# Performance work log

Hardware: AMD Instinct MI355X
Metric: run time of the kernel (lower is better)

## Reference

```python
import jax, jax.numpy as jnp
import numpy as np

N, E, G = 20000, 320000, 128
L, D, De, Fa, Ff = 3, 64, 32, 92, 128
IN = 2 * D + De  # 160


def setup_inputs() -> dict:
    key = jax.random.key(0)
    ks = jax.random.split(key, 12)
    s = 0.05
    return {
        "atom_features": jax.random.normal(ks[0], (N, Fa), jnp.float32),
        "bondlength": jax.random.uniform(ks[1], (E,), jnp.float32) * 8.0,
        "src": jax.random.randint(ks[2], (E,), 0, N, dtype=jnp.int32),
        "dst": jax.random.randint(ks[3], (E,), 0, N, dtype=jnp.int32),
        "graph_id": jnp.sort(jax.random.randint(ks[4], (N,), 0, G, dtype=jnp.int32)),
        "emb_W": jax.random.normal(ks[5], (Fa, D), jnp.float32) * s,
        "emb_b": jnp.zeros((D,), jnp.float32),
        "Wi": jax.random.normal(ks[6], (L, IN, D), jnp.float32) * s,
        "bi": jnp.zeros((L, D), jnp.float32),
        "gi": jnp.ones((L, D), jnp.float32),
        "bbi": jnp.zeros((L, D), jnp.float32),
        "Wu": jax.random.normal(ks[7], (L, IN, D), jnp.float32) * s,
        "bu": jnp.zeros((L, D), jnp.float32),
        "gu": jnp.ones((L, D), jnp.float32),
        "bbu": jnp.zeros((L, D), jnp.float32),
        "gn": jnp.ones((L, D), jnp.float32),
        "bbn": jnp.zeros((L, D), jnp.float32),
        "fc_W": jax.random.normal(ks[8], (D, Ff), jnp.float32) * s,
        "fc_b": jnp.zeros((Ff,), jnp.float32),
        "out_W": jax.random.normal(ks[9], (Ff, 1), jnp.float32) * s,
        "out_b": jnp.zeros((1,), jnp.float32),
    }


def _bn(x, g, b, eps=1e-5):
    # BatchNorm1d in training mode: biased batch statistics over axis 0
    mu = x.mean(axis=0)
    var = x.var(axis=0)
    return g * (x - mu) * jax.lax.rsqrt(var + eps) + b


def _rbf(d):
    centers = jnp.linspace(0.0, 8.0, De)
    gamma = 1.0 / (8.0 / (De - 1))  # 1 / mean center spacing (alignn default)
    return jnp.exp(-gamma * (d[:, None] - centers) ** 2)  # [E, De]


def reference(atom_features, bondlength, src, dst, graph_id,
              emb_W, emb_b, Wi, bi, gi, bbi, Wu, bu, gu, bbu, gn, bbn,
              fc_W, fc_b, out_W, out_b):
    sp = jax.nn.softplus
    edge_feats = _rbf(bondlength)                       # [E, De]
    h = atom_features @ emb_W + emb_b                   # [N, D]
    for l in range(L):
        z = jnp.concatenate([h[src], h[dst], edge_feats], axis=1)  # [E, 160]
        gate = jax.nn.sigmoid(_bn(z @ Wi[l] + bi[l], gi[l], bbi[l]))
        upd = sp(_bn(z @ Wu[l] + bu[l], gu[l], bbu[l]))
        m = jax.ops.segment_sum(gate * upd, dst, num_segments=N)   # [N, D]
        h = sp(h + _bn(m, gn[l], bbn[l]))
    # AvgPooling over graphs
    sums = jax.ops.segment_sum(h, graph_id, num_segments=G)       # [G, D]
    cnt = jax.ops.segment_sum(jnp.ones((N,), h.dtype), graph_id, num_segments=G)
    feats = sums / jnp.maximum(cnt, 1.0)[:, None]
    feats = sp(feats)
    feats = sp(feats @ fc_W + fc_b)   # Linear + Softplus (self.fc)
    feats = sp(feats)
    out = feats @ out_W + out_b       # [G, 1], identity link
    return jnp.squeeze(out, axis=-1)  # [G]
```

## Files before the change

kernel.cpp:

```cpp
#include <hip/hip_runtime.h>
#include <hip/hip_bf16.h>
#include <math.h>

#define NN 20000
#define NE 320000
#define NG 128
#define DD 64
#define FA 92
#define FF 128
#define NT (NE / 16)
#define NBLK 2500
#define NAB 1250
#define NHB 625
#define GAMMA 3.875f
#define CEN (8.0f / 31.0f)
#define L2E 1.44269504f
#define RBF2 (-GAMMA * L2E)

typedef __attribute__((ext_vector_type(8))) short bf16x8;
typedef __attribute__((ext_vector_type(4))) float f32x4;


__device__ __forceinline__ float sp_(float x) {
    return fmaxf(x, 0.f) + __logf(1.f + __expf(-fabsf(x)));
}
__device__ __forceinline__ unsigned short f2b(float x) {
    __hip_bfloat16 b = __float2bfloat16(x);
    return *reinterpret_cast<unsigned short*>(&b);
}
__device__ __forceinline__ float b2f(unsigned short u) {
    return __uint_as_float((unsigned)u << 16);
}

__device__ __forceinline__ float tree16(float v[16], int r) {
#pragma unroll
    for (int m = 1; m < 16; m <<= 1) {
        bool b = (r & m) != 0;
        int cnt = 8 / m;
#pragma unroll
        for (int i = 0; i < cnt; ++i) {
            float keep = b ? v[2 * i + 1] : v[2 * i];
            float disc = b ? v[2 * i] : v[2 * i + 1];
            float recv = __shfl_xor(disc, m, 64);
            v[i] = keep + recv;
        }
    }
    return v[0];
}

__global__ __launch_bounds__(256) void embed_k(const float* __restrict__ af,
                                               const float* __restrict__ W,
                                               const float* __restrict__ b,
                                               float* __restrict__ h,
                                               unsigned short* __restrict__ hb) {
    __shared__ float Ws[FA * DD];
    __shared__ float afS[32][FA];
    const int n0 = blockIdx.x * 32;
    for (int i = threadIdx.x * 4; i < FA * DD; i += 256 * 4)
        *(float4*)&Ws[i] = *(const float4*)&W[i];
    const float4* af4 = (const float4*)(af + (size_t)n0 * FA);
    for (int i = threadIdx.x; i < 32 * FA / 4; i += 256) {
        float4 v = af4[i];
        int nl = i / (FA / 4), kk = (i % (FA / 4)) * 4;
        *(float4*)&afS[nl][kk] = v;
    }
    __syncthreads();
    int nl = threadIdx.x >> 3, ch = threadIdx.x & 7;
    int n = n0 + nl;
    float acc[8];
#pragma unroll
    for (int q = 0; q < 8; ++q) acc[q] = b[ch * 8 + q];
#pragma unroll 4
    for (int k = 0; k < FA; ++k) {
        float a = afS[nl][k];
        const float* wr = &Ws[k * DD + ch * 8];
        float4 w0 = *(const float4*)wr;
        float4 w1 = *(const float4*)(wr + 4);
        acc[0] += a * w0.x; acc[1] += a * w0.y; acc[2] += a * w0.z; acc[3] += a * w0.w;
        acc[4] += a * w1.x; acc[5] += a * w1.y; acc[6] += a * w1.z; acc[7] += a * w1.w;
    }
    float* o = h + (size_t)n * DD + ch * 8;
    float4 o0, o1;
    o0.x = acc[0]; o0.y = acc[1]; o0.z = acc[2]; o0.w = acc[3];
    o1.x = acc[4]; o1.y = acc[5]; o1.z = acc[6]; o1.w = acc[7];
    *(float4*)o = o0;
    *(float4*)(o + 4) = o1;
    bf16x8 hb8;
#pragma unroll
    for (int q = 0; q < 8; ++q) hb8[q] = (short)f2b(acc[q]);
    *(bf16x8*)(hb + (size_t)n * DD + ch * 8) = hb8;
}

__global__ void prep_wf_k(const float* __restrict__ Wi, const float* __restrict__ Wu,
                          unsigned short* __restrict__ Wf) {
    int b = blockIdx.x;
    int l = b >> 1, g = b & 1;
    const float* W = (g ? Wu : Wi) + (size_t)l * 160 * DD;
    for (int f = threadIdx.x; f < 10240; f += 256) {
        int i = f & 7;
        int lane = (f >> 3) & 63;
        int nf = (f >> 9) & 3;
        int kt = f >> 11;
        int k = kt * 32 + 8 * (lane >> 4) + i;
        int col = nf * 16 + (lane & 15);
        Wf[(size_t)b * 10240 + f] = f2b(W[k * DD + col]);
    }
}

__global__ void cnt_edges_k(const int* __restrict__ src, const int* __restrict__ dst,
                            int* __restrict__ icnt, int* __restrict__ ocnt) {
    int e = blockIdx.x * 256 + threadIdx.x;
    if (e < NE) {
        atomicAdd(&icnt[dst[e]], 1);
        atomicAdd(&ocnt[src[e]], 1);
    }
}

__global__ __launch_bounds__(1024) void csr_scan_k(const int* __restrict__ cnt,
                                                   int* __restrict__ off,
                                                   int* __restrict__ cur) {
    __shared__ int part[1024];
    int t = threadIdx.x;
    int base = t * 20;
    int s = 0;
    for (int i = 0; i < 20; ++i) { int idx = base + i; if (idx < NN) s += cnt[idx]; }
    part[t] = s;
    __syncthreads();
    for (int ofs = 1; ofs < 1024; ofs <<= 1) {
        int v = (t >= ofs) ? part[t - ofs] : 0;
        __syncthreads();
        part[t] += v;
        __syncthreads();
    }
    int run = (t == 0) ? 0 : part[t - 1];
    for (int i = 0; i < 20; ++i) {
        int idx = base + i;
        if (idx < NN) { off[idx] = run; cur[idx] = run; run += cnt[idx]; }
    }
    if (t == 1023) off[NN] = run;
}

__global__ void fill_edges_k(const int* __restrict__ src, const int* __restrict__ dst,
                             const float* __restrict__ bond,
                             int* __restrict__ cur, int* __restrict__ ssrc,
                             int* __restrict__ sdst, float* __restrict__ bond_s) {
    int e = blockIdx.x * 256 + threadIdx.x;
    if (e < NE) {
        int d = dst[e];
        int p = atomicAdd(&cur[d], 1);
        ssrc[p] = src[e];
        sdst[p] = d;
        bond_s[p] = bond[e];
    }
}

__global__ __launch_bounds__(256) void rbfsum_k(const float* __restrict__ bond,
                                                float* __restrict__ zr) {
    __shared__ float part[4][32];
    int lane = threadIdx.x & 63;
    int w = threadIdx.x >> 6;
    int col = lane & 31;
    int half = lane >> 5;
    int slot = (blockIdx.x * 4 + w) * 2 + half;
    int nslots = gridDim.x * 8;
    float cen = (float)col * CEN;
    float a = 0.f;
    for (int e = slot; e < NE; e += nslots) {
        float u = bond[e] - cen;
        a += b2f(f2b(__builtin_amdgcn_exp2f(u * u * RBF2)));
    }
    a += __shfl_xor(a, 32, 64);
    if (half == 0) part[w][col] = a;
    __syncthreads();
    if (threadIdx.x < 32) {
        float s = part[0][threadIdx.x] + part[1][threadIdx.x] +
                  part[2][threadIdx.x] + part[3][threadIdx.x];
        unsafeAtomicAdd(&zr[threadIdx.x], s);
    }
}

__global__ __launch_bounds__(256) void zsum_node_k(const unsigned short* __restrict__ hb,
                                                   const int* __restrict__ ocnt,
                                                   const int* __restrict__ icnt,
                                                   float* __restrict__ zS,
                                                   float* __restrict__ zD) {
    int t = blockIdx.x * 256 + threadIdx.x;
    int col = t & 63;
    int n0 = t >> 6;
    int nstride = (gridDim.x * 256) >> 6;
    float aS = 0.f, aD = 0.f;
    for (int n = n0; n < NN; n += nstride) {
        float v = b2f(hb[(size_t)n * DD + col]);
        aS += (float)ocnt[n] * v;
        aD += (float)icnt[n] * v;
    }
    unsafeAtomicAdd(&zS[col], aS);
    unsafeAtomicAdd(&zD[col], aD);
}

__global__ __launch_bounds__(512, 8) void edge_pre3_k(const unsigned short* __restrict__ hb,
                                                      const float* __restrict__ bond_s,
                                                      const unsigned short* __restrict__ Wf,
                                                      const int* __restrict__ ssrc,
                                                      const int* __restrict__ sdst,
                                                      unsigned short* __restrict__ preIb,
                                                      unsigned short* __restrict__ preUb,
                                                      float* __restrict__ pq) {
    __shared__ bf16x8 WfS[2560];
    float* qred = (float*)WfS;
    const int bidx = blockIdx.x;
    const int lane = threadIdx.x & 63;
    const int w = threadIdx.x >> 6;
    const int r = lane & 15;
    const int c = lane >> 4;
    const int tile = bidx * 8 + w;
    const int e = tile * 16 + r;

    int es = ssrc[e];
    int ed = sdst[e];
    float bd = bond_s[e];
    bf16x8 a0 = *(const bf16x8*)(hb + (size_t)es * DD + c * 8);
    bf16x8 a1 = *(const bf16x8*)(hb + (size_t)es * DD + 32 + c * 8);
    bf16x8 a2 = *(const bf16x8*)(hb + (size_t)ed * DD + c * 8);
    bf16x8 a3 = *(const bf16x8*)(hb + (size_t)ed * DD + 32 + c * 8);
    bf16x8 a4;
#pragma unroll
    for (int i = 0; i < 8; ++i) {
        float u = bd - (float)(8 * c + i) * CEN;
        a4[i] = (short)f2b(__builtin_amdgcn_exp2f(u * u * RBF2));
    }

    {
        const bf16x8* Wf8 = (const bf16x8*)Wf;
        for (int i = threadIdx.x; i < 2560; i += 512) WfS[i] = Wf8[i];
    }
    __syncthreads();

    float qI[16], qU[16];
    {
        f32x4 acc[4];
#pragma unroll
        for (int nf = 0; nf < 4; ++nf) { f32x4 z4 = {0.f, 0.f, 0.f, 0.f}; acc[nf] = z4; }
#pragma unroll
        for (int kt = 0; kt < 5; ++kt) {
            bf16x8 a = (kt == 0) ? a0 : (kt == 1) ? a1 : (kt == 2) ? a2 : (kt == 3) ? a3 : a4;
#pragma unroll
            for (int nf = 0; nf < 4; ++nf)
                acc[nf] = __builtin_amdgcn_mfma_f32_16x16x32_bf16(WfS[(kt * 4 + nf) * 64 + lane], a, acc[nf], 0, 0, 0);
        }
        unsigned short* pre = preIb + (size_t)e * DD + c * 4;
#pragma unroll
        for (int nf = 0; nf < 4; ++nf) {
            ushort4 o;
            o.x = f2b(acc[nf][0]); o.y = f2b(acc[nf][1]);
            o.z = f2b(acc[nf][2]); o.w = f2b(acc[nf][3]);
            *(ushort4*)(pre + nf * 16) = o;
#pragma unroll
            for (int j = 0; j < 4; ++j) qI[nf * 4 + j] = acc[nf][j] * acc[nf][j];
        }
    }
    {
        f32x4 acc[4];
#pragma unroll
        for (int nf = 0; nf < 4; ++nf) { f32x4 z4 = {0.f, 0.f, 0.f, 0.f}; acc[nf] = z4; }
#pragma unroll
        for (int kt = 0; kt < 5; ++kt) {
            bf16x8 a = (kt == 0) ? a0 : (kt == 1) ? a1 : (kt == 2) ? a2 : (kt == 3) ? a3 : a4;
#pragma unroll
            for (int nf = 0; nf < 4; ++nf)
                acc[nf] = __builtin_amdgcn_mfma_f32_16x16x32_bf16(WfS[1280 + (kt * 4 + nf) * 64 + lane], a, acc[nf], 0, 0, 0);
        }
        unsigned short* pre = preUb + (size_t)e * DD + c * 4;
#pragma unroll
        for (int nf = 0; nf < 4; ++nf) {
            ushort4 o;
            o.x = f2b(acc[nf][0]); o.y = f2b(acc[nf][1]);
            o.z = f2b(acc[nf][2]); o.w = f2b(acc[nf][3]);
            *(ushort4*)(pre + nf * 16) = o;
#pragma unroll
            for (int j = 0; j < 4; ++j) qU[nf * 4 + j] = acc[nf][j] * acc[nf][j];
        }
    }

    float vI = tree16(qI, r);
    float vU = tree16(qU, r);
    int col = (r >> 2) * 16 + c * 4 + (r & 3);
    __syncthreads();
    qred[w * 128 + col] = vI;
    qred[w * 128 + 64 + col] = vU;
    __syncthreads();
    if (threadIdx.x < 128) {
        float s8 = 0.f;
#pragma unroll
        for (int ww = 0; ww < 8; ++ww) s8 += qred[ww * 128 + threadIdx.x];
        pq[(size_t)threadIdx.x * NBLK + bidx] = s8;
    }
}

__global__ __launch_bounds__(256) void red2_k(const float* __restrict__ pq,
                                              const float* __restrict__ zpart,
                                              float* __restrict__ stats, int withz) {
    __shared__ float red[256];
    int b = blockIdx.x;
    const float* row;
    float* out;
    int len;
    if (b < 128) { row = pq + (size_t)b * NBLK; out = &stats[b]; len = NBLK; }
    else {
        if (!withz) return;
        row = zpart + (size_t)(b - 128) * NHB; out = &stats[256 + (b - 128)]; len = NHB;
    }
    float s = 0.f;
    for (int i = threadIdx.x; i < len; i += 256) s += row[i];
    red[threadIdx.x] = s;
    __syncthreads();
    for (int ofs = 128; ofs >= 1; ofs >>= 1) {
        if (threadIdx.x < ofs) red[threadIdx.x] += red[threadIdx.x + ofs];
        __syncthreads();
    }
    if (threadIdx.x == 0) *out = red[0];
}

__global__ __launch_bounds__(256) void fin_iu_k(const float* __restrict__ stats,
                                                const unsigned short* __restrict__ Wf,
                                                const float* __restrict__ gi, const float* __restrict__ bbi,
                                                const float* __restrict__ gu, const float* __restrict__ bbu,
                                                float* __restrict__ coeff) {
    __shared__ float redI[256], redU[256];
    int t = threadIdx.x;
    int j = t & 63, part = t >> 6;
    int nf = j >> 4, rr = j & 15;
    float muI = 0.f, muU = 0.f;
    for (int k = part; k < 160; k += 4) {
        float zs = (k < 128) ? stats[256 + k] : stats[384 + k - 128];
        int kt = k >> 5, rem = k & 31, cc = rem >> 3, ii = rem & 7;
        int f = kt * 2048 + nf * 512 + (cc * 16 + rr) * 8 + ii;
        muI += zs * b2f(Wf[f]);
        muU += zs * b2f(Wf[10240 + f]);
    }
    redI[t] = muI;
    redU[t] = muU;
    __syncthreads();
    if (t < 64) {
        muI = redI[t] + redI[64 + t] + redI[128 + t] + redI[192 + t];
        muU = redU[t] + redU[64 + t] + redU[128 + t] + redU[192 + t];
        const float invE = 1.f / (float)NE;
        muI *= invE; muU *= invE;
        float varI = stats[t] * invE - muI * muI;
        float sI = gi[t] * rsqrtf(varI + 1e-5f);
        float tI = bbi[t] - muI * sI;
        float varU = stats[64 + t] * invE - muU * muU;
        float sU = gu[t] * rsqrtf(varU + 1e-5f);
        float tU = bbu[t] - muU * sU;
        coeff[t]       = -L2E * sI;
        coeff[64 + t]  = -L2E * tI;
        coeff[128 + t] =  L2E * sU;
        coeff[192 + t] =  L2E * tU;
    }
}

__global__ __launch_bounds__(256) void apply_node_k(const unsigned short* __restrict__ preIb,
                                                    const unsigned short* __restrict__ preUb,
                                                    const int* __restrict__ eoff,
                                                    const float* __restrict__ coeff,
                                                    float* __restrict__ m,
                                                    float* __restrict__ mpart) {
    __shared__ float ps[128][8];
    __shared__ float pq2[128][8];
    int ch = threadIdx.x & 7;
    int half = (threadIdx.x >> 3) & 1;
    int nl = threadIdx.x >> 4;
    int n = blockIdx.x * 16 + nl;
    float sIv[8], tIv[8], sUv[8], tUv[8];
#pragma unroll
    for (int q = 0; q < 8; ++q) {
        int col = ch * 8 + q;
        sIv[q] = coeff[col];       tIv[q] = coeff[64 + col];
        sUv[q] = coeff[128 + col]; tUv[q] = coeff[192 + col];
    }
    int b = eoff[n], e = eoff[n + 1];
    float acc[8];
#pragma unroll
    for (int q = 0; q < 8; ++q) acc[q] = 0.f;
    for (int p = b + half; p < e; p += 2) {
        bf16x8 vi = *(const bf16x8*)(preIb + (size_t)p * DD + ch * 8);
        bf16x8 vu = *(const bf16x8*)(preUb + (size_t)p * DD + ch * 8);
#pragma unroll
        for (int q = 0; q < 8; ++q) {
            float xi = fmaf(b2f((unsigned short)vi[q]), sIv[q], tIv[q]);
            float den = 1.f + __builtin_amdgcn_exp2f(xi);
            float xu = fmaf(b2f((unsigned short)vu[q]), sUv[q], tUv[q]);
            float lu = __builtin_amdgcn_logf(1.f + __builtin_amdgcn_exp2f(xu));
            acc[q] = fmaf(lu, __builtin_amdgcn_rcpf(den), acc[q]);
        }
    }
#pragma unroll
    for (int q = 0; q < 8; ++q) acc[q] += __shfl_xor(acc[q], 8, 64);
    if (half == 0) {
        float* mp = m + (size_t)n * DD + ch * 8;
        float4 v0, v1;
        v0.x = acc[0]; v0.y = acc[1]; v0.z = acc[2]; v0.w = acc[3];
        v1.x = acc[4]; v1.y = acc[5]; v1.z = acc[6]; v1.w = acc[7];
        *(float4*)mp = v0;
        *(float4*)(mp + 4) = v1;
        int idx = nl * 8 + ch;
#pragma unroll
        for (int q = 0; q < 8; ++q) {
            ps[idx][q] = acc[q];
            pq2[idx][q] = acc[q] * acc[q];
        }
    }
    __syncthreads();
    if (threadIdx.x < 64) {
        int j = threadIdx.x;
        int chh = j >> 3, qq = j & 7;
        float s = 0.f, q2 = 0.f;
#pragma unroll
        for (int nn = 0; nn < 16; ++nn) {
            s += ps[nn * 8 + chh][qq];
            q2 += pq2[nn * 8 + chh][qq];
        }
        mpart[(size_t)j * NAB + blockIdx.x] = s;
        mpart[(size_t)(64 + j) * NAB + blockIdx.x] = q2;
    }
}

__global__ __launch_bounds__(256) void fin_n3_k(const float* __restrict__ mpart,
                                                const float* __restrict__ gn,
                                                const float* __restrict__ bbn,
                                                float* __restrict__ coeffN) {
    __shared__ float red1[256], red2[256];
    int j = blockIdx.x;
    float s1 = 0.f, s2 = 0.f;
    for (int i = threadIdx.x; i < NAB; i += 256) {
        s1 += mpart[(size_t)j * NAB + i];
        s2 += mpart[(size_t)(64 + j) * NAB + i];
    }
    red1[threadIdx.x] = s1;
    red2[threadIdx.x] = s2;
    __syncthreads();
    for (int ofs = 128; ofs >= 1; ofs >>= 1) {
        if (threadIdx.x < ofs) {
            red1[threadIdx.x] += red1[threadIdx.x + ofs];
            red2[threadIdx.x] += red2[threadIdx.x + ofs];
        }
        __syncthreads();
    }
    if (threadIdx.x == 0) {
        const float invN = 1.f / (float)NN;
        float mu = red1[0] * invN;
        float var = red2[0] * invN - mu * mu;
        float sc = gn[j] * rsqrtf(var + 1e-5f);
        coeffN[j] = sc;
        coeffN[64 + j] = bbn[j] - mu * sc;
    }
}

__global__ __launch_bounds__(256) void h_update_k(float* __restrict__ h,
                                                  unsigned short* __restrict__ hb,
                                                  const float* __restrict__ m,
                                                  const float* __restrict__ coeffN,
                                                  const int* __restrict__ ocnt,
                                                  const int* __restrict__ icnt,
                                                  float* __restrict__ zpart,
                                                  int fin) {
    __shared__ float wzs[4][8][8], wzd[4][8][8];
    int t = blockIdx.x * 256 + threadIdx.x;
    int n = t >> 3, ch = t & 7;
    int base = n * DD + ch * 8;
    float4 m0 = *(const float4*)(m + base);
    float4 m1 = *(const float4*)(m + base + 4);
    float4 h0 = *(const float4*)(h + base);
    float4 h1 = *(const float4*)(h + base + 4);
    float mv[8] = {m0.x, m0.y, m0.z, m0.w, m1.x, m1.y, m1.z, m1.w};
    float hv[8] = {h0.x, h0.y, h0.z, h0.w, h1.x, h1.y, h1.z, h1.w};
    unsigned short hbv[8];
#pragma unroll
    for (int q = 0; q < 8; ++q) {
        int col = ch * 8 + q;
        float v = sp_(hv[q] + mv[q] * coeffN[col] + coeffN[64 + col]);
        hv[q] = v;
        hbv[q] = f2b(v);
    }
    float4 o0, o1;
    o0.x = hv[0]; o0.y = hv[1]; o0.z = hv[2]; o0.w = hv[3];
    o1.x = hv[4]; o1.y = hv[5]; o1.z = hv[6]; o1.w = hv[7];
    *(float4*)(h + base) = o0;
    *(float4*)(h + base + 4) = o1;
    if (fin) return;

    bf16x8 hb8;
#pragma unroll
    for (int q = 0; q < 8; ++q) hb8[q] = (short)hbv[q];
    *(bf16x8*)(hb + base) = hb8;

    float oc = (float)ocnt[n], ic = (float)icnt[n];
    float zs8[8], zd8[8];
#pragma unroll
    for (int q = 0; q < 8; ++q) {
        float r = b2f(hbv[q]);
        zs8[q] = r * oc;
        zd8[q] = r * ic;
    }
#pragma unroll
    for (int mk = 8; mk <= 32; mk <<= 1) {
#pragma unroll
        for (int q = 0; q < 8; ++q) {
            zs8[q] += __shfl_xor(zs8[q], mk, 64);
            zd8[q] += __shfl_xor(zd8[q], mk, 64);
        }
    }
    int lane = threadIdx.x & 63;
    int w = threadIdx.x >> 6;
    if (lane < 8) {
#pragma unroll
        for (int q = 0; q < 8; ++q) {
            wzs[w][lane][q] = zs8[q];
            wzd[w][lane][q] = zd8[q];
        }
    }
    __syncthreads();
    if (threadIdx.x < 64) {
        int chh = threadIdx.x >> 3, qq = threadIdx.x & 7;
        float s = wzs[0][chh][qq] + wzs[1][chh][qq] + wzs[2][chh][qq] + wzs[3][chh][qq];
        float d = wzd[0][chh][qq] + wzd[1][chh][qq] + wzd[2][chh][qq] + wzd[3][chh][qq];
        zpart[(size_t)threadIdx.x * NHB + blockIdx.x] = s;
        zpart[(size_t)(64 + threadIdx.x) * NHB + blockIdx.x] = d;
    }
}

__global__ __launch_bounds__(256) void pool_seg_k(const float* __restrict__ h,
                                                  const int* __restrict__ gid,
                                                  float* __restrict__ pool,
                                                  float* __restrict__ pcnt) {
    __shared__ int s_lo, s_hi;
    __shared__ float red[4][DD];
    int g = blockIdx.x;
    if (threadIdx.x == 0) {
        int lo = 0, hi = NN;
        while (lo < hi) { int mid = (lo + hi) >> 1; if (gid[mid] < g) lo = mid + 1; else hi = mid; }
        s_lo = lo;
        int lo2 = lo, hi2 = NN;
        while (lo2 < hi2) { int mid = (lo2 + hi2) >> 1; if (gid[mid] < g + 1) lo2 = mid + 1; else hi2 = mid; }
        s_hi = lo2;
    }
    __syncthreads();
    int lo = s_lo, hi = s_hi;
    int col = threadIdx.x & 63;
    int rr = threadIdx.x >> 6;
    float s = 0.f;
    for (int n = lo + rr; n < hi; n += 4) s += h[(size_t)n * DD + col];
    red[rr][col] = s;
    __syncthreads();
    if (threadIdx.x < 64) {
        float v = red[0][col] + red[1][col] + red[2][col] + red[3][col];
        pool[(size_t)g * DD + col] = v;
        if (col == 0) pcnt[g] = (float)(hi - lo);
    }
}

__global__ __launch_bounds__(128) void head_k(const float* __restrict__ pool,
                                              const float* __restrict__ pcnt,
                                              const float* __restrict__ fcW,
                                              const float* __restrict__ fcb,
                                              const float* __restrict__ oW,
                                              const float* __restrict__ ob,
                                              float* __restrict__ out) {
    int g = blockIdx.x;
    int t = threadIdx.x;
    __shared__ float feats[DD];
    __shared__ float red[FF];
    if (t < DD) {
        float c = fmaxf(pcnt[g], 1.f);
        feats[t] = sp_(pool[(size_t)g * DD + t] / c);
    }
    __syncthreads();
    float a = fcb[t];
#pragma unroll 1
    for (int j = 0; j < DD; ++j) a += feats[j] * fcW[j * FF + t];
    float y = sp_(sp_(a));
    red[t] = y * oW[t];
    __syncthreads();
    for (int s2 = 64; s2 >= 1; s2 >>= 1) {
        if (t < s2) red[t] += red[t + s2];
        __syncthreads();
    }
    if (t == 0) out[g] = red[0] + ob[0];
}

extern "C" void kernel_launch(void* const* d_in, const int* in_sizes, int n_in,
                              void* d_out, int out_size, void* d_ws, size_t ws_size,
                              hipStream_t stream) {
    const float* af   = (const float*)d_in[0];
    const float* bond = (const float*)d_in[1];
    const int*   src  = (const int*)d_in[2];
    const int*   dst  = (const int*)d_in[3];
    const int*   gid  = (const int*)d_in[4];
    const float* embW = (const float*)d_in[5];
    const float* embB = (const float*)d_in[6];
    const float* Wi   = (const float*)d_in[7];
    const float* gi   = (const float*)d_in[9];
    const float* bbi  = (const float*)d_in[10];
    const float* Wu   = (const float*)d_in[11];
    const float* gu   = (const float*)d_in[13];
    const float* bbu  = (const float*)d_in[14];
    const float* gn   = (const float*)d_in[15];
    const float* bbn  = (const float*)d_in[16];
    const float* fcW  = (const float*)d_in[17];
    const float* fcb  = (const float*)d_in[18];
    const float* oW   = (const float*)d_in[19];
    const float* ob   = (const float*)d_in[20];
    float* out = (float*)d_out;

    char* ws = (char*)d_ws;
    size_t off = 0;
    auto take = [&](size_t bytes) {
        size_t o = off;
        off += (bytes + 255) & ~(size_t)255;
        return o;
    };
    float* h     = (float*)(ws + take((size_t)NN * DD * 4));
    float* m     = (float*)(ws + take((size_t)NN * DD * 4));
    float* stats = (float*)(ws + take(512 * 4));
    float* coeff = (float*)(ws + take(512 * 4));
    float* pq    = (float*)(ws + take((size_t)128 * NBLK * 4));
    float* mpart = (float*)(ws + take((size_t)128 * NAB * 4));
    float* zpart = (float*)(ws + take((size_t)128 * NHB * 4));
    float* pool  = (float*)(ws + take((size_t)NG * DD * 4));
    float* pcnt  = (float*)(ws + take((size_t)NG * 4));
    int* ecount  = (int*)(ws + take((size_t)NN * 4));
    int* ocount  = (int*)(ws + take((size_t)NN * 4));
    int* eoff    = (int*)(ws + take((size_t)(NN + 1) * 4));
    int* ecur    = (int*)(ws + take((size_t)NN * 4));
    int* ssrc    = (int*)(ws + take((size_t)NE * 4));
    int* sdst    = (int*)(ws + take((size_t)NE * 4));
    float* bond_s = (float*)(ws + take((size_t)NE * 4));
    unsigned short* hb    = (unsigned short*)(ws + take((size_t)NN * DD * 2));
    unsigned short* preIb = (unsigned short*)(ws + take((size_t)NE * DD * 2));
    unsigned short* preUb = (unsigned short*)(ws + take((size_t)NE * DD * 2));
    unsigned short* Wf    = (unsigned short*)(ws + take((size_t)6 * 10240 * 2));

    hipMemsetAsync((void*)ecount, 0, 2 * (((size_t)NN * 4 + 255) & ~(size_t)255), stream);
    hipMemsetAsync((void*)stats, 0, 512 * 4, stream);

    prep_wf_k<<<6, 256, 0, stream>>>(Wi, Wu, Wf);
    embed_k<<<NN / 32, 256, 0, stream>>>(af, embW, embB, h, hb);

    cnt_edges_k<<<(NE + 255) / 256, 256, 0, stream>>>(src, dst, ecount, ocount);
    csr_scan_k<<<1, 1024, 0, stream>>>(ecount, eoff, ecur);
    fill_edges_k<<<(NE + 255) / 256, 256, 0, stream>>>(src, dst, bond, ecur, ssrc, sdst, bond_s);
    rbfsum_k<<<512, 256, 0, stream>>>(bond, stats + 384);
    zsum_node_k<<<128, 256, 0, stream>>>(hb, ocount, ecount, stats + 256, stats + 320);

    for (int l = 0; l < 3; ++l) {
        const unsigned short* Wfl = Wf + (size_t)l * 2 * 10240;
        edge_pre3_k<<<NBLK, 512, 0, stream>>>(hb, bond_s, Wfl, ssrc, sdst, preIb, preUb, pq);
        red2_k<<<256, 256, 0, stream>>>(pq, zpart, stats, l > 0 ? 1 : 0);
        fin_iu_k<<<1, 256, 0, stream>>>(stats, Wfl, gi + l * DD, bbi + l * DD,
                                        gu + l * DD, bbu + l * DD, coeff);
        apply_node_k<<<NAB, 256, 0, stream>>>(preIb, preUb, eoff, coeff, m, mpart);
        fin_n3_k<<<64, 256, 0, stream>>>(mpart, gn + l * DD, bbn + l * DD, coeff + 256);
        h_update_k<<<NHB, 256, 0, stream>>>(h, hb, m, coeff + 256, ocount, ecount,
                                            zpart, l == 2 ? 1 : 0);
    }

    pool_seg_k<<<NG, 256, 0, stream>>>(h, gid, pool, pcnt);
    head_k<<<NG, 128, 0, stream>>>(pool, pcnt, fcW, fcb, oW, ob, out);
}
```

Before: 435.7 us.

## Stage edge pre-activations through LDS for coalesced stores and merge setup kernels

The edge MFMA kernel now writes its bf16 results for each 16-edge tile into a padded LDS slot, reads them back, and writes them to global memory as contiguous 16-element chunks per lane instead of scattered 4-element stores. It reuses the weight LDS buffer after a barrier, which adds LDS traffic and an extra sync in exchange for fully coalesced global writes of the two large pre-activation arrays. Separately, the weight-prep kernel is folded into the embedding launch as extra blocks, and the RBF and node z-sum reductions are merged into one launch. Those two merges are meant to save launch overhead.

```diff
diff --git a/kernel.cpp b/kernel.cpp
--- a/kernel.cpp
+++ b/kernel.cpp
@@ -52,7 +52,25 @@
                                                const float* __restrict__ W,
                                                const float* __restrict__ b,
                                                float* __restrict__ h,
-                                               unsigned short* __restrict__ hb) {
+                                               unsigned short* __restrict__ hb,
+                                               const float* __restrict__ Wi,
+                                               const float* __restrict__ Wu,
+                                               unsigned short* __restrict__ Wf) {
+    if (blockIdx.x >= NN / 32) {
+        int bb = blockIdx.x - NN / 32;
+        int l = bb >> 1, g = bb & 1;
+        const float* Wsrc = (g ? Wu : Wi) + (size_t)l * 160 * DD;
+        for (int f = threadIdx.x; f < 10240; f += 256) {
+            int i = f & 7;
+            int lane = (f >> 3) & 63;
+            int nf = (f >> 9) & 3;
+            int kt = f >> 11;
+            int k = kt * 32 + 8 * (lane >> 4) + i;
+            int col = nf * 16 + (lane & 15);
+            Wf[(size_t)bb * 10240 + f] = f2b(Wsrc[k * DD + col]);
+        }
+        return;
+    }
     __shared__ float Ws[FA * DD];
     __shared__ float afS[32][FA];
     const int n0 = blockIdx.x * 32;
@@ -89,22 +107,6 @@
 #pragma unroll
     for (int q = 0; q < 8; ++q) hb8[q] = (short)f2b(acc[q]);
     *(bf16x8*)(hb + (size_t)n * DD + ch * 8) = hb8;
-}
-
-__global__ void prep_wf_k(const float* __restrict__ Wi, const float* __restrict__ Wu,
-                          unsigned short* __restrict__ Wf) {
-    int b = blockIdx.x;
-    int l = b >> 1, g = b & 1;
-    const float* W = (g ? Wu : Wi) + (size_t)l * 160 * DD;
-    for (int f = threadIdx.x; f < 10240; f += 256) {
-        int i = f & 7;
-        int lane = (f >> 3) & 63;
-        int nf = (f >> 9) & 3;
-        int kt = f >> 11;
-        int k = kt * 32 + 8 * (lane >> 4) + i;
-        int col = nf * 16 + (lane & 15);
-        Wf[(size_t)b * 10240 + f] = f2b(W[k * DD + col]);
-    }
 }
 
 __global__ void cnt_edges_k(const int* __restrict__ src, const int* __restrict__ dst,
@@ -154,48 +156,50 @@
     }
 }
 
-__global__ __launch_bounds__(256) void rbfsum_k(const float* __restrict__ bond,
-                                                float* __restrict__ zr) {
-    __shared__ float part[4][32];
-    int lane = threadIdx.x & 63;
-    int w = threadIdx.x >> 6;
-    int col = lane & 31;
-    int half = lane >> 5;
-    int slot = (blockIdx.x * 4 + w) * 2 + half;
-    int nslots = gridDim.x * 8;
-    float cen = (float)col * CEN;
-    float a = 0.f;
-    for (int e = slot; e < NE; e += nslots) {
-        float u = bond[e] - cen;
-        a += b2f(f2b(__builtin_amdgcn_exp2f(u * u * RBF2)));
-    }
-    a += __shfl_xor(a, 32, 64);
-    if (half == 0) part[w][col] = a;
-    __syncthreads();
-    if (threadIdx.x < 32) {
-        float s = part[0][threadIdx.x] + part[1][threadIdx.x] +
-                  part[2][threadIdx.x] + part[3][threadIdx.x];
-        unsafeAtomicAdd(&zr[threadIdx.x], s);
-    }
-}
-
-__global__ __launch_bounds__(256) void zsum_node_k(const unsigned short* __restrict__ hb,
-                                                   const int* __restrict__ ocnt,
-                                                   const int* __restrict__ icnt,
-                                                   float* __restrict__ zS,
-                                                   float* __restrict__ zD) {
-    int t = blockIdx.x * 256 + threadIdx.x;
-    int col = t & 63;
-    int n0 = t >> 6;
-    int nstride = (gridDim.x * 256) >> 6;
-    float aS = 0.f, aD = 0.f;
-    for (int n = n0; n < NN; n += nstride) {
-        float v = b2f(hb[(size_t)n * DD + col]);
-        aS += (float)ocnt[n] * v;
-        aD += (float)icnt[n] * v;
-    }
-    unsafeAtomicAdd(&zS[col], aS);
-    unsafeAtomicAdd(&zD[col], aD);
+__global__ __launch_bounds__(256) void rbfzsum_k(const float* __restrict__ bond,
+                                                 const unsigned short* __restrict__ hb,
+                                                 const int* __restrict__ ocnt,
+                                                 const int* __restrict__ icnt,
+                                                 float* __restrict__ zr,
+                                                 float* __restrict__ zS,
+                                                 float* __restrict__ zD) {
+    if (blockIdx.x < 512) {
+        __shared__ float part[4][32];
+        int lane = threadIdx.x & 63;
+        int w = threadIdx.x >> 6;
+        int col = lane & 31;
+        int half = lane >> 5;
+        int slot = (blockIdx.x * 4 + w) * 2 + half;
+        int nslots = 512 * 8;
+        float cen = (float)col * CEN;
+        float a = 0.f;
+        for (int e = slot; e < NE; e += nslots) {
+            float u = bond[e] - cen;
+            a += b2f(f2b(__builtin_amdgcn_exp2f(u * u * RBF2)));
+        }
+        a += __shfl_xor(a, 32, 64);
+        if (half == 0) part[w][col] = a;
+        __syncthreads();
+        if (threadIdx.x < 32) {
+            float s = part[0][threadIdx.x] + part[1][threadIdx.x] +
+                      part[2][threadIdx.x] + part[3][threadIdx.x];
+            unsafeAtomicAdd(&zr[threadIdx.x], s);
+        }
+    } else {
+        int bb = blockIdx.x - 512;
+        int t = bb * 256 + threadIdx.x;
+        int col = t & 63;
+        int n0 = t >> 6;
+        int nstride = (128 * 256) >> 6;
+        float aS = 0.f, aD = 0.f;
+        for (int n = n0; n < NN; n += nstride) {
+            float v = b2f(hb[(size_t)n * DD + col]);
+            aS += (float)ocnt[n] * v;
+            aD += (float)icnt[n] * v;
+        }
+        unsafeAtomicAdd(&zS[col], aS);
+        unsafeAtomicAdd(&zD[col], aD);
+    }
 }
 
 __global__ __launch_bounds__(512, 8) void edge_pre3_k(const unsigned short* __restrict__ hb,
@@ -207,6 +211,7 @@
                                                       unsigned short* __restrict__ preUb,
                                                       float* __restrict__ pq) {
     __shared__ bf16x8 WfS[2560];
+    unsigned short* tbuf = (unsigned short*)WfS;
     float* qred = (float*)WfS;
     const int bidx = blockIdx.x;
     const int lane = threadIdx.x & 63;
@@ -237,6 +242,39 @@
     __syncthreads();
 
     float qI[16], qU[16];
+    f32x4 accI[4];
+    {
+#pragma unroll
+        for (int nf = 0; nf < 4; ++nf) { f32x4 z4 = {0.f, 0.f, 0.f, 0.f}; accI[nf] = z4; }
+#pragma unroll
+        for (int kt = 0; kt < 5; ++kt) {
+            bf16x8 a = (kt == 0) ? a0 : (kt == 1) ? a1 : (kt == 2) ? a2 : (kt == 3) ? a3 : a4;
+#pragma unroll
+            for (int nf = 0; nf < 4; ++nf)
+                accI[nf] = __builtin_amdgcn_mfma_f32_16x16x32_bf16(WfS[(kt * 4 + nf) * 64 + lane], a, accI[nf], 0, 0, 0);
+        }
+#pragma unroll
+        for (int nf = 0; nf < 4; ++nf)
+#pragma unroll
+            for (int j = 0; j < 4; ++j) qI[nf * 4 + j] = accI[nf][j] * accI[nf][j];
+    }
+    __syncthreads();
+
+    unsigned short* slot = tbuf + w * 1152;
+    {
+#pragma unroll
+        for (int nf = 0; nf < 4; ++nf) {
+            ushort4 o;
+            o.x = f2b(accI[nf][0]); o.y = f2b(accI[nf][1]);
+            o.z = f2b(accI[nf][2]); o.w = f2b(accI[nf][3]);
+            *(ushort4*)(slot + r * 72 + c * 4 + nf * 16) = o;
+        }
+        bf16x8 v0 = *(const bf16x8*)(slot + (lane >> 2) * 72 + (lane & 3) * 16);
+        bf16x8 v1 = *(const bf16x8*)(slot + (lane >> 2) * 72 + (lane & 3) * 16 + 8);
+        unsigned short* dst0 = preIb + (size_t)tile * 1024 + lane * 16;
+        *(bf16x8*)dst0 = v0;
+        *(bf16x8*)(dst0 + 8) = v1;
+    }
     {
         f32x4 acc[4];
 #pragma unroll
@@ -246,40 +284,22 @@
             bf16x8 a = (kt == 0) ? a0 : (kt == 1) ? a1 : (kt == 2) ? a2 : (kt == 3) ? a3 : a4;
 #pragma unroll
             for (int nf = 0; nf < 4; ++nf)
-                acc[nf] = __builtin_amdgcn_mfma_f32_16x16x32_bf16(WfS[(kt * 4 + nf) * 64 + lane], a, acc[nf], 0, 0, 0);
-        }
-        unsigned short* pre = preIb + (size_t)e * DD + c * 4;
+                acc[nf] = __builtin_amdgcn_mfma_f32_16x16x32_bf16(WfS[1280 + (kt * 4 + nf) * 64 + lane], a, acc[nf], 0, 0, 0);
+        }
 #pragma unroll
         for (int nf = 0; nf < 4; ++nf) {
             ushort4 o;
             o.x = f2b(acc[nf][0]); o.y = f2b(acc[nf][1]);
             o.z = f2b(acc[nf][2]); o.w = f2b(acc[nf][3]);
-            *(ushort4*)(pre + nf * 16) = o;
-#pragma unroll
-            for (int j = 0; j < 4; ++j) qI[nf * 4 + j] = acc[nf][j] * acc[nf][j];
-        }
-    }
-    {
-        f32x4 acc[4];
-#pragma unroll
-        for (int nf = 0; nf < 4; ++nf) { f32x4 z4 = {0.f, 0.f, 0.f, 0.f}; acc[nf] = z4; }
-#pragma unroll
-        for (int kt = 0; kt < 5; ++kt) {
-            bf16x8 a = (kt == 0) ? a0 : (kt == 1) ? a1 : (kt == 2) ? a2 : (kt == 3) ? a3 : a4;
-#pragma unroll
-            for (int nf = 0; nf < 4; ++nf)
-                acc[nf] = __builtin_amdgcn_mfma_f32_16x16x32_bf16(WfS[1280 + (kt * 4 + nf) * 64 + lane], a, acc[nf], 0, 0, 0);
-        }
-        unsigned short* pre = preUb + (size_t)e * DD + c * 4;
-#pragma unroll
-        for (int nf = 0; nf < 4; ++nf) {
-            ushort4 o;
-            o.x = f2b(acc[nf][0]); o.y = f2b(acc[nf][1]);
-            o.z = f2b(acc[nf][2]); o.w = f2b(acc[nf][3]);
-            *(ushort4*)(pre + nf * 16) = o;
+            *(ushort4*)(slot + r * 72 + c * 4 + nf * 16) = o;
 #pragma unroll
             for (int j = 0; j < 4; ++j) qU[nf * 4 + j] = acc[nf][j] * acc[nf][j];
         }
+        bf16x8 v0 = *(const bf16x8*)(slot + (lane >> 2) * 72 + (lane & 3) * 16);
+        bf16x8 v1 = *(const bf16x8*)(slot + (lane >> 2) * 72 + (lane & 3) * 16 + 8);
+        unsigned short* dst0 = preUb + (size_t)tile * 1024 + lane * 16;
+        *(bf16x8*)dst0 = v0;
+        *(bf16x8*)(dst0 + 8) = v1;
     }
 
     float vI = tree16(qI, r);
@@ -643,14 +663,13 @@
     hipMemsetAsync((void*)ecount, 0, 2 * (((size_t)NN * 4 + 255) & ~(size_t)255), stream);
     hipMemsetAsync((void*)stats, 0, 512 * 4, stream);
 
-    prep_wf_k<<<6, 256, 0, stream>>>(Wi, Wu, Wf);
-    embed_k<<<NN / 32, 256, 0, stream>>>(af, embW, embB, h, hb);
+    embed_k<<<NN / 32 + 6, 256, 0, stream>>>(af, embW, embB, h, hb, Wi, Wu, Wf);
 
     cnt_edges_k<<<(NE + 255) / 256, 256, 0, stream>>>(src, dst, ecount, ocount);
     csr_scan_k<<<1, 1024, 0, stream>>>(ecount, eoff, ecur);
     fill_edges_k<<<(NE + 255) / 256, 256, 0, stream>>>(src, dst, bond, ecur, ssrc, sdst, bond_s);
-    rbfsum_k<<<512, 256, 0, stream>>>(bond, stats + 384);
-    zsum_node_k<<<128, 256, 0, stream>>>(hb, ocount, ecount, stats + 256, stats + 320);
+    rbfzsum_k<<<640, 256, 0, stream>>>(bond, hb, ocount, ecount, stats + 384, stats + 256,
+                                       stats + 320);
 
     for (int l = 0; l < 3; ++l) {
         const unsigned short* Wfl = Wf + (size_t)l * 2 * 10240;
```

Measured after the change: 400.0 us. 1.09x faster.
